# Optimization experiments

Hardware: AMD Instinct MI355X
Metric: run time of the kernel (lower is better)

The kernel has to match this reference:

```python
import jax, jax.numpy as jnp
import numpy as np


def _pointnet(x, w1, b1, w2, b2, w3, b3):
    # x: [B, 3, P]; shared per-point MLP 3->64->128->128, max-pool over points -> [B,128]
    h = jax.nn.relu(jnp.einsum('oc,bcp->bop', w1, x) + b1[None, :, None])
    h = jax.nn.relu(jnp.einsum('oc,bcp->bop', w2, h) + b2[None, :, None])
    h = jax.nn.relu(jnp.einsum('oc,bcp->bop', w3, h) + b3[None, :, None])
    return h.max(axis=2)


def _lstm_layer(x, wih, whh, b):
    # x: [B, T, D]; standard LSTM (pytorch gate order i,f,g,o), returns [B, T, 128]
    B = x.shape[0]
    h0 = jnp.zeros((B, 128), x.dtype)
    def step(carry, xt):
        h, c = carry
        g = xt @ wih.T + h @ whh.T + b
        i, f, gg, o = jnp.split(g, 4, axis=-1)
        c = jax.nn.sigmoid(f) * c + jax.nn.sigmoid(i) * jnp.tanh(gg)
        h = jax.nn.sigmoid(o) * jnp.tanh(c)
        return (h, c), h
    _, hs = jax.lax.scan(step, (h0, h0), jnp.swapaxes(x, 0, 1))
    return jnp.swapaxes(hs, 0, 1)


def _edgeconv(x, aff, tw, tb, pw, pb, N):
    # DGL EdgeConv, max aggregation. Edges: det i -> track (N+j) where aff[i,j]==1, plus
    # self loops on every node. Message on edge u->v: theta(x_u - x_v) + phi(x_v).
    phi = x @ pw.T + pb                                   # [N+M, 256]
    diff = x[:N][:, None, :] - x[N:][None, :, :]          # [N, M, 256] (x_src - x_dst)
    msg = jnp.einsum('nmc,oc->nmo', diff, tw) + tb        # theta applied to diffs
    msg = jnp.where(aff[:, :, None] > 0, msg, jnp.finfo(x.dtype).min)
    h_trk = phi[N:] + jnp.maximum(tb, msg.max(axis=0))    # self-loop message is theta(0)=tb
    h_det = phi[:N] + tb                                  # dets only receive their self loop
    return jnp.concatenate([h_det, h_trk], axis=0)


def _forward(det_pc_in_box, det_boxes3d, track_pc_in_box, track_boxes3d, init_aff_matrix,
             pn_w1, pn_b1, pn_w2, pn_b2, pn_w3, pn_b3,
             mlp_w1, mlp_b1, mlp_w2, mlp_b2,
             l0_wih, l0_whh, l0_b, l1_wih, l1_whh, l1_b,
             ec_tw, ec_tb, ec_pw, ec_pb,
             er_w1, er_b1, er_w2, er_b2):
    N = det_pc_in_box.shape[0]
    det_app = _pointnet(jnp.swapaxes(det_pc_in_box, 1, 2), pn_w1, pn_b1, pn_w2, pn_b2, pn_w3, pn_b3)
    trk_app = _pointnet(jnp.swapaxes(track_pc_in_box, 1, 2), pn_w1, pn_b1, pn_w2, pn_b2, pn_w3, pn_b3)
    det_mot = jax.nn.relu(det_boxes3d @ mlp_w1.T + mlp_b1) @ mlp_w2.T + mlp_b2
    trk_mot = _lstm_layer(_lstm_layer(track_boxes3d, l0_wih, l0_whh, l0_b), l1_wih, l1_whh, l1_b)[:, -1, :]
    h = jnp.concatenate([jnp.concatenate([det_app, det_mot], axis=1),
                         jnp.concatenate([trk_app, trk_mot], axis=1)], axis=0)  # [N+M, 256]
    for k in range(4):
        h = jax.nn.relu(_edgeconv(h, init_aff_matrix, ec_tw[k], ec_tb[k], ec_pw[k], ec_pb[k], N))
    # pairwise affinity: (track - det) differences through small MLP + sigmoid (BCE head)
    edges = h[N:][None, :, :] - h[:N][:, None, :]                                # [N, M, 256]
    e = jax.nn.relu(jnp.einsum('nmc,oc->nmo', edges, er_w1) + er_b1)             # [N, M, 64]
    regr = jax.nn.sigmoid(jnp.einsum('nmo,ko->nmk', e, er_w2) + er_b2)[..., 0]   # [N, M]
    valid = init_aff_matrix * regr
    valid = jnp.where(valid == 0, jnp.asarray(99.0, valid.dtype), valid)
    return valid


def setup_inputs() -> dict:
    key = jax.random.key(0)
    ks = jax.random.split(key, 20)
    N, M, P, T = 512, 512, 256, 10
    f = jnp.float32
    def rn(k, shp):
        return jax.random.normal(k, shp, dtype=f) * 0.05
    return {
        'det_pc_in_box': jax.random.normal(ks[0], (N, P, 3), dtype=f),
        'det_boxes3d': jax.random.normal(ks[1], (N, 9), dtype=f),
        'track_pc_in_box': jax.random.normal(ks[2], (M, P, 3), dtype=f),
        'track_boxes3d': jax.random.normal(ks[3], (M, T, 9), dtype=f),
        'init_aff_matrix': jnp.ones((N, M), dtype=f),
        'gt_affinity_matrix': jnp.zeros((N, M), dtype=jnp.int32),
        'pn_w1': rn(ks[4], (64, 3)), 'pn_b1': jnp.zeros((64,), f),
        'pn_w2': rn(ks[5], (128, 64)), 'pn_b2': jnp.zeros((128,), f),
        'pn_w3': rn(ks[6], (128, 128)), 'pn_b3': jnp.zeros((128,), f),
        'mlp_w1': rn(ks[7], (64, 9)), 'mlp_b1': jnp.zeros((64,), f),
        'mlp_w2': rn(ks[8], (128, 64)), 'mlp_b2': jnp.zeros((128,), f),
        'l0_wih': rn(ks[9], (512, 9)), 'l0_whh': rn(ks[10], (512, 128)), 'l0_b': jnp.zeros((512,), f),
        'l1_wih': rn(ks[11], (512, 128)), 'l1_whh': rn(ks[12], (512, 128)), 'l1_b': jnp.zeros((512,), f),
        'ec_tw': rn(ks[13], (4, 256, 256)), 'ec_tb': jnp.zeros((4, 256), f),
        'ec_pw': rn(ks[14], (4, 256, 256)), 'ec_pb': jnp.zeros((4, 256), f),
        'er_w1': rn(ks[15], (64, 256)), 'er_b1': jnp.zeros((64,), f),
        'er_w2': rn(ks[16], (1, 64)), 'er_b2': jnp.zeros((1,), f),
    }


def reference(det_pc_in_box, det_boxes3d, track_pc_in_box, track_boxes3d, init_aff_matrix,
              gt_affinity_matrix,
              pn_w1, pn_b1, pn_w2, pn_b2, pn_w3, pn_b3,
              mlp_w1, mlp_b1, mlp_w2, mlp_b2,
              l0_wih, l0_whh, l0_b, l1_wih, l1_whh, l1_b,
              ec_tw, ec_tb, ec_pw, ec_pb,
              er_w1, er_b1, er_w2, er_b2):
    # gt_affinity_matrix is only used by the training loss; inference path ignores it.
    return _forward(det_pc_in_box, det_boxes3d, track_pc_in_box, track_boxes3d, init_aff_matrix,
                    pn_w1, pn_b1, pn_w2, pn_b2, pn_w3, pn_b3,
                    mlp_w1, mlp_b1, mlp_w2, mlp_b2,
                    l0_wih, l0_whh, l0_b, l1_wih, l1_whh, l1_b,
                    ec_tw, ec_tb, ec_pw, ec_pb,
                    er_w1, er_b1, er_w2, er_b2)
```

## Files before the change

kernel.cpp:

```cpp
#include <hip/hip_runtime.h>
#include <math.h>

#define N_DET 512
#define N_TRK 512
#define NPTS  256

typedef __attribute__((ext_vector_type(8))) short short8;
typedef __attribute__((ext_vector_type(4))) float f32x4;

__device__ __forceinline__ float sigm(float x) { return 1.f / (1.f + expf(-x)); }

__device__ __forceinline__ unsigned short f2bf(float f) {
    unsigned u = __float_as_uint(f);
    u += 0x7FFF + ((u >> 16) & 1);
    return (unsigned short)(u >> 16);
}

__global__ __launch_bounds__(64) void pn_wprep_kernel(
    const float* __restrict__ w2, const float* __restrict__ w3,
    unsigned short* __restrict__ wfrag)
{
    const int f = blockIdx.x;
    const int lane = threadIdx.x;
    const int lm = lane & 15, lg = lane >> 4;
    const float* src;
    if (f < 16) {
        const int s = f >> 3, n = f & 7;
        src = w2 + (size_t)(n*16 + lm)*64 + s*32 + lg*8;
    } else {
        const int f2 = f - 16, s = f2 >> 3, n = f2 & 7;
        src = w3 + (size_t)(n*16 + lm)*128 + s*32 + lg*8;
    }
    short8 v;
#pragma unroll
    for (int j = 0; j < 8; ++j) v[j] = (short)f2bf(src[j]);
    *reinterpret_cast<short8*>(wfrag + ((size_t)f*64 + lane)*8) = v;
}

__global__ __launch_bounds__(256, 1) void pointnet_mfma_kernel(
    const float* __restrict__ det_pc, const float* __restrict__ trk_pc,
    const float* __restrict__ w1, const float* __restrict__ b1,
    const unsigned short* __restrict__ wfrag,
    const float* __restrict__ b2, const float* __restrict__ b3,
    float* __restrict__ hout)
{
    __shared__ unsigned short h1s[256*72];
    __shared__ unsigned short h2s[256*136];
    __shared__ float wmaxs[4][128];

    const int tid = threadIdx.x;
    const int box = blockIdx.x;
    const int lane = tid & 63, w = tid >> 6;
    const int lm = lane & 15, lg = lane >> 4;

    const float* pc = (box < N_DET) ? det_pc + ((size_t)box*NPTS + tid)*3
                                    : trk_pc + ((size_t)(box - N_DET)*NPTS + tid)*3;
    const float x = pc[0], y = pc[1], z = pc[2];
#pragma unroll
    for (int j = 0; j < 8; ++j) {
        short8 v;
#pragma unroll
        for (int o = 0; o < 8; ++o) {
            const int ch = j*8 + o;
            float s = fmaf(w1[ch*3+0], x, fmaf(w1[ch*3+1], y,
                        fmaf(w1[ch*3+2], z, b1[ch])));
            v[o] = (short)f2bf(fmaxf(s, 0.f));
        }
        *reinterpret_cast<short8*>(&h1s[tid*72 + j*8]) = v;
    }
    __syncthreads();

    short8 w2f[16];
#pragma unroll
    for (int f = 0; f < 16; ++f)
        w2f[f] = *reinterpret_cast<const short8*>(wfrag + ((size_t)f*64 + lane)*8);
    float b2v[8];
#pragma unroll
    for (int n = 0; n < 8; ++n) b2v[n] = b2[n*16 + lm];

#pragma unroll
    for (int t = 0; t < 4; ++t) {
        const int arow = w*64 + t*16 + lm;
        const short8 a0 = *reinterpret_cast<const short8*>(&h1s[arow*72 + lg*8]);
        const short8 a1 = *reinterpret_cast<const short8*>(&h1s[arow*72 + 32 + lg*8]);
        const int wrow = w*64 + t*16 + lg*4;
#pragma unroll
        for (int n = 0; n < 8; ++n) {
            f32x4 acc = {0.f, 0.f, 0.f, 0.f};
            acc = __builtin_amdgcn_mfma_f32_16x16x32_bf16(a0, w2f[n],     acc, 0, 0, 0);
            acc = __builtin_amdgcn_mfma_f32_16x16x32_bf16(a1, w2f[8 + n], acc, 0, 0, 0);
#pragma unroll
            for (int r = 0; r < 4; ++r) {
                const float v = fmaxf(acc[r] + b2v[n], 0.f);
                h2s[(wrow + r)*136 + n*16 + lm] = f2bf(v);
            }
        }
    }
    __syncthreads();

    short8 w3f[32];
#pragma unroll
    for (int f = 0; f < 32; ++f)
        w3f[f] = *reinterpret_cast<const short8*>(wfrag + ((size_t)(16 + f)*64 + lane)*8);

    float pm[8];
#pragma unroll
    for (int n = 0; n < 8; ++n) pm[n] = -3.0e38f;

#pragma unroll
    for (int t = 0; t < 4; ++t) {
        const int arow = w*64 + t*16 + lm;
        const short8 a0 = *reinterpret_cast<const short8*>(&h2s[arow*136 +  0 + lg*8]);
        const short8 a1 = *reinterpret_cast<const short8*>(&h2s[arow*136 + 32 + lg*8]);
        const short8 a2 = *reinterpret_cast<const short8*>(&h2s[arow*136 + 64 + lg*8]);
        const short8 a3 = *reinterpret_cast<const short8*>(&h2s[arow*136 + 96 + lg*8]);
#pragma unroll
        for (int n = 0; n < 8; ++n) {
            f32x4 acc = {0.f, 0.f, 0.f, 0.f};
            acc = __builtin_amdgcn_mfma_f32_16x16x32_bf16(a0, w3f[n],      acc, 0, 0, 0);
            acc = __builtin_amdgcn_mfma_f32_16x16x32_bf16(a1, w3f[8 + n],  acc, 0, 0, 0);
            acc = __builtin_amdgcn_mfma_f32_16x16x32_bf16(a2, w3f[16 + n], acc, 0, 0, 0);
            acc = __builtin_amdgcn_mfma_f32_16x16x32_bf16(a3, w3f[24 + n], acc, 0, 0, 0);
#pragma unroll
            for (int r = 0; r < 4; ++r) pm[n] = fmaxf(pm[n], acc[r]);
        }
    }
#pragma unroll
    for (int n = 0; n < 8; ++n) {
        float v = pm[n];
        v = fmaxf(v, __shfl_xor(v, 16, 64));
        v = fmaxf(v, __shfl_xor(v, 32, 64));
        pm[n] = v;
    }
    if (lg == 0) {
#pragma unroll
        for (int n = 0; n < 8; ++n) wmaxs[w][n*16 + lm] = pm[n];
    }
    __syncthreads();
    if (tid < 128) {
        const float m = fmaxf(fmaxf(wmaxs[0][tid], wmaxs[1][tid]),
                              fmaxf(wmaxs[2][tid], wmaxs[3][tid]));
        hout[(size_t)box*256 + tid] = fmaxf(m + b3[tid], 0.f);
    }
}

__global__ __launch_bounds__(128) void detmlp_kernel(
    const float* __restrict__ boxes,
    const float* __restrict__ w1, const float* __restrict__ b1,
    const float* __restrict__ w2, const float* __restrict__ b2,
    float* __restrict__ hout)
{
    __shared__ float xb[9];
    __shared__ float h1[64];
    const int b = blockIdx.x, t = threadIdx.x;
    if (t < 9) xb[t] = boxes[b*9 + t];
    __syncthreads();
    if (t < 64) {
        float s = b1[t];
#pragma unroll
        for (int c = 0; c < 9; ++c) s = fmaf(w1[t*9+c], xb[c], s);
        h1[t] = fmaxf(s, 0.f);
    }
    __syncthreads();
    float s = b2[t];
    const float* wr = w2 + t*64;
#pragma unroll
    for (int c = 0; c < 64; ++c) s = fmaf(wr[c], h1[c], s);
    hout[(size_t)b * 256 + 128 + t] = s;
}

__global__ __launch_bounds__(256) void transpose_wih1_kernel(
    const float* __restrict__ in, float* __restrict__ out)
{
    const int id = blockIdx.x * 256 + threadIdx.x;
    const int k = id >> 9, r = id & 511;
    out[id] = in[r * 128 + k];
}

__global__ __launch_bounds__(512) void lstm_rec0_kernel(
    const float* __restrict__ xseq,
    const float* __restrict__ wih0, const float* __restrict__ whh0,
    const float* __restrict__ b0, float* __restrict__ h0seq)
{
    __shared__ float hs[128][2];
    __shared__ float xb[2][12];
    __shared__ float gs[4][2][128];
    const int r  = threadIdx.x;
    const int b2 = blockIdx.x * 2;
    const int q  = r >> 7 & 3, jj = r & 127;
    const int mb = r >> 7, mj = r & 127;

    float w[128];
#pragma unroll
    for (int k = 0; k < 128; k += 4) {
        const float4 v = *(const float4*)(whh0 + (size_t)r * 128 + k);
        w[k] = v.x; w[k+1] = v.y; w[k+2] = v.z; w[k+3] = v.w;
    }
    float wx[9];
#pragma unroll
    for (int c = 0; c < 9; ++c) wx[c] = wih0[(size_t)r * 9 + c];
    const float bias = b0[r];

    float cst = 0.f;
    if (r < 256) hs[mj][mb] = 0.f;
    __syncthreads();

    for (int t = 0; t < 10; ++t) {
        if (r < 18) xb[r / 9][r % 9] = xseq[((size_t)(b2 + r / 9) * 10 + t) * 9 + r % 9];
        __syncthreads();
        float a0 = bias, a1 = bias;
#pragma unroll
        for (int c = 0; c < 9; ++c) {
            a0 = fmaf(wx[c], xb[0][c], a0);
            a1 = fmaf(wx[c], xb[1][c], a1);
        }
#pragma unroll
        for (int k = 0; k < 128; ++k) {
            const float2 h2 = *(const float2*)&hs[k][0];
            a0 = fmaf(w[k], h2.x, a0);
            a1 = fmaf(w[k], h2.y, a1);
        }
        gs[q][0][jj] = a0;
        gs[q][1][jj] = a1;
        __syncthreads();
        if (r < 256) {
            const float gi = gs[0][mb][mj], gf = gs[1][mb][mj];
            const float gg = gs[2][mb][mj], go = gs[3][mb][mj];
            cst = sigm(gf) * cst + sigm(gi) * tanhf(gg);
            const float hn = sigm(go) * tanhf(cst);
            hs[mj][mb] = hn;
            h0seq[((size_t)(b2 + mb) * 10 + t) * 128 + mj] = hn;
        }
        __syncthreads();
    }
}

__global__ __launch_bounds__(512) void lstm_rec1_kernel(
    const float* __restrict__ h0seq, const float* __restrict__ wih1T,
    const float* __restrict__ whh1, const float* __restrict__ b1,
    float* __restrict__ hout)
{
    __shared__ float hs[128][2];
    __shared__ float xs_[128][2];
    __shared__ float gs[4][2][128];
    const int r  = threadIdx.x;
    const int b2 = blockIdx.x * 2;
    const int q  = r >> 7 & 3, jj = r & 127;
    const int mb = r >> 7, mj = r & 127;

    float w[128];
#pragma unroll
    for (int k = 0; k < 128; k += 4) {
        const float4 v = *(const float4*)(whh1 + (size_t)r * 128 + k);
        w[k] = v.x; w[k+1] = v.y; w[k+2] = v.z; w[k+3] = v.w;
    }
    const float bias = b1[r];

    float cst = 0.f;
    if (r < 256) hs[mj][mb] = 0.f;
    __syncthreads();

    for (int t = 0; t < 10; ++t) {
        if (r < 256)
            xs_[mj][mb] = h0seq[((size_t)(b2 + mb) * 10 + t) * 128 + mj];
        __syncthreads();
        float a0 = bias, a1 = bias;
#pragma unroll
        for (int k = 0; k < 128; ++k) {
            const float wxv = wih1T[k * 512 + r];
            const float2 x2 = *(const float2*)&xs_[k][0];
            const float2 h2 = *(const float2*)&hs[k][0];
            a0 = fmaf(wxv, x2.x, fmaf(w[k], h2.x, a0));
            a1 = fmaf(wxv, x2.y, fmaf(w[k], h2.y, a1));
        }
        gs[q][0][jj] = a0;
        gs[q][1][jj] = a1;
        __syncthreads();
        if (r < 256) {
            const float gi = gs[0][mb][mj], gf = gs[1][mb][mj];
            const float gg = gs[2][mb][mj], go = gs[3][mb][mj];
            cst = sigm(gf) * cst + sigm(gi) * tanhf(gg);
            const float hn = sigm(go) * tanhf(cst);
            hs[mj][mb] = hn;
            if (t == 9)
                hout[(size_t)(N_DET + b2 + mb) * 256 + 128 + mj] = hn;
        }
        __syncthreads();
    }
}

__global__ __launch_bounds__(256) void ec_gemm_kernel(
    const float* __restrict__ hin,
    const float* __restrict__ tw, const float* __restrict__ tb,
    const float* __restrict__ pw, const float* __restrict__ pb,
    float* __restrict__ Abuf, float* __restrict__ Bbuf,
    float* __restrict__ phiT, float* __restrict__ hnext)
{
    __shared__ float As[16][68];
    __shared__ float Ws[16][68];
    const int bm = blockIdx.x, bn = blockIdx.y;
    const int tid = threadIdx.x;
    const int tx = tid & 15, ty = tid >> 4;
    float acc[4][4] = {};
    for (int kk = 0; kk < 256; kk += 16) {
        if (kk) __syncthreads();
#pragma unroll
        for (int i = 0; i < 4; ++i) {
            const int e = tid + 256*i;
            const int r = e >> 4, c = e & 15;
            As[c][r] = hin[(size_t)(bm*64 + r)*256 + kk + c];
            const int n = bn*64 + r;
            const float* wp = (n < 256) ? (tw + (size_t)n*256) : (pw + (size_t)(n-256)*256);
            Ws[c][r] = wp[kk + c];
        }
        __syncthreads();
#pragma unroll
        for (int k = 0; k < 16; ++k) {
            const float4 a = *(const float4*)&As[k][ty*4];
            const float4 w = *(const float4*)&Ws[k][tx*4];
            const float av[4] = {a.x, a.y, a.z, a.w};
            const float wv[4] = {w.x, w.y, w.z, w.w};
#pragma unroll
            for (int i = 0; i < 4; ++i)
#pragma unroll
                for (int jj = 0; jj < 4; ++jj)
                    acc[i][jj] = fmaf(av[i], wv[jj], acc[i][jj]);
        }
    }
    const int row0 = bm*64 + ty*4;
    const int col0 = bn*64 + tx*4;
#pragma unroll
    for (int i = 0; i < 4; ++i) {
#pragma unroll
        for (int jj = 0; jj < 4; ++jj) {
            const int row = row0 + i, col = col0 + jj;
            float v = acc[i][jj];
            if (col < 256) {
                if (row < N_DET) Abuf[(size_t)row*256 + col] = v;
                else             Bbuf[(size_t)(row - N_DET)*256 + col] = v;
            } else {
                const int o = col - 256;
                v += pb[o];
                if (row < N_DET) hnext[(size_t)row*256 + o] = fmaxf(v + tb[o], 0.f);
                else             phiT[(size_t)(row - N_DET)*256 + o] = v;
            }
        }
    }
}

#define CM_MT 16
#define CM_OT 32
#define CM_NC 64

__global__ __launch_bounds__(256) void ec_colmax_kernel(
    const float* __restrict__ aff,
    const float* __restrict__ Abuf, const float* __restrict__ Bbuf,
    const float* __restrict__ phiT, const float* __restrict__ tb,
    float* __restrict__ hnext)
{
    __shared__ float As[CM_NC][CM_OT + 4];
    __shared__ float Fs[CM_NC][CM_MT + 4];
    const int t = threadIdx.x;
    const int mtile = blockIdx.x;
    const int otile = blockIdx.y;
    const int mi = t >> 4, oi = t & 15;

    float mx0 = -3.0e38f, mx1 = -3.0e38f;

    for (int n0 = 0; n0 < 512; n0 += CM_NC) {
        if (n0) __syncthreads();
        {
            const int r = t >> 3, c4 = (t & 7) * 4;
#pragma unroll
            for (int rr = 0; rr < 2; ++rr) {
                const float4 v = *(const float4*)(
                    Abuf + (size_t)(n0 + rr*32 + r)*256 + otile*CM_OT + c4);
                *(float4*)&As[rr*32 + r][c4] = v;
            }
        }
        {
            const int n = t >> 2, m4 = (t & 3) * 4;
            const float4 a = *(const float4*)(
                aff + (size_t)(n0 + n)*512 + mtile*CM_MT + m4);
            float4 f;
            f.x = (a.x > 0.f) ? 0.f : -3.0e38f;
            f.y = (a.y > 0.f) ? 0.f : -3.0e38f;
            f.z = (a.z > 0.f) ? 0.f : -3.0e38f;
            f.w = (a.w > 0.f) ? 0.f : -3.0e38f;
            *(float4*)&Fs[n][m4] = f;
        }
        __syncthreads();
#pragma unroll 4
        for (int n = 0; n < CM_NC; ++n) {
            const float f = Fs[n][mi];
            const float2 a = *(const float2*)&As[n][oi*2];
            mx0 = fmaxf(mx0, a.x + f);
            mx1 = fmaxf(mx1, a.y + f);
        }
    }

    const int m = mtile*CM_MT + mi;
    const int o = otile*CM_OT + oi*2;
    const float2 tb2 = *(const float2*)(tb + o);
    const float2 bb  = *(const float2*)(Bbuf + (size_t)m*256 + o);
    const float2 ph  = *(const float2*)(phiT + (size_t)m*256 + o);
    const float v0 = fmaxf(tb2.x, mx0 - bb.x + tb2.x);
    const float v1 = fmaxf(tb2.y, mx1 - bb.y + tb2.y);
    float2 outv;
    outv.x = fmaxf(ph.x + v0, 0.f);
    outv.y = fmaxf(ph.y + v1, 0.f);
    *(float2*)(hnext + (size_t)(N_DET + m)*256 + o) = outv;
}

__global__ __launch_bounds__(256) void headp_kernel(
    const float* __restrict__ h, const float* __restrict__ w1, float* __restrict__ P)
{
    const int tid = threadIdx.x;
    const int o = tid & 63, rl = tid >> 6;
    const int row = blockIdx.x * 4 + rl;
    const float* hr = h + (size_t)row * 256;
    const float* wr = w1 + (size_t)o * 256;
    float s0 = 0.f, s1 = 0.f, s2 = 0.f, s3 = 0.f;
#pragma unroll
    for (int c = 0; c < 256; c += 4) {
        const float4 hv = *(const float4*)(hr + c);
        const float4 wv = *(const float4*)(wr + c);
        s0 = fmaf(hv.x, wv.x, s0);
        s1 = fmaf(hv.y, wv.y, s1);
        s2 = fmaf(hv.z, wv.z, s2);
        s3 = fmaf(hv.w, wv.w, s3);
    }
    P[(size_t)row * 64 + o] = (s0 + s1) + (s2 + s3);
}

__global__ __launch_bounds__(256) void pairwise_kernel(
    const float* __restrict__ P, const float* __restrict__ aff,
    const float* __restrict__ eb1, const float* __restrict__ ew2, const float* __restrict__ eb2,
    float* __restrict__ out)
{
    __shared__ float pd[64], sb1[64], sw2[64];
    const int n = blockIdx.y;
    const int t = threadIdx.x;
    if (t < 64)       pd[t]        = P[(size_t)n * 64 + t];
    else if (t < 128) sb1[t - 64]  = eb1[t - 64];
    else if (t < 192) sw2[t - 128] = ew2[t - 128];
    __syncthreads();
    const int m = blockIdx.x * 256 + t;
    const float* pt = P + (size_t)(N_DET + m) * 64;
    float s = eb2[0];
#pragma unroll
    for (int c = 0; c < 64; c += 4) {
        const float4 pv = *(const float4*)(pt + c);
        float e;
        e = fmaxf(pv.x - pd[c+0] + sb1[c+0], 0.f); s = fmaf(e, sw2[c+0], s);
        e = fmaxf(pv.y - pd[c+1] + sb1[c+1], 0.f); s = fmaf(e, sw2[c+1], s);
        e = fmaxf(pv.z - pd[c+2] + sb1[c+2], 0.f); s = fmaf(e, sw2[c+2], s);
        e = fmaxf(pv.w - pd[c+3] + sb1[c+3], 0.f); s = fmaf(e, sw2[c+3], s);
    }
    const float r = 1.f / (1.f + expf(-s));
    const float v = aff[(size_t)n * 512 + m] * r;
    out[(size_t)n * 512 + m] = (v == 0.f) ? 99.f : v;
}

extern "C" void kernel_launch(void* const* d_in, const int* in_sizes, int n_in,
                              void* d_out, int out_size, void* d_ws, size_t ws_size,
                              hipStream_t stream)
{
    (void)in_sizes; (void)n_in; (void)out_size; (void)ws_size;

    const float* det_pc  = (const float*)d_in[0];
    const float* det_box = (const float*)d_in[1];
    const float* trk_pc  = (const float*)d_in[2];
    const float* trk_box = (const float*)d_in[3];
    const float* aff     = (const float*)d_in[4];
    const float* pn_w1  = (const float*)d_in[6];
    const float* pn_b1  = (const float*)d_in[7];
    const float* pn_w2  = (const float*)d_in[8];
    const float* pn_b2  = (const float*)d_in[9];
    const float* pn_w3  = (const float*)d_in[10];
    const float* pn_b3  = (const float*)d_in[11];
    const float* mlp_w1 = (const float*)d_in[12];
    const float* mlp_b1 = (const float*)d_in[13];
    const float* mlp_w2 = (const float*)d_in[14];
    const float* mlp_b2 = (const float*)d_in[15];
    const float* l0_wih = (const float*)d_in[16];
    const float* l0_whh = (const float*)d_in[17];
    const float* l0_b   = (const float*)d_in[18];
    const float* l1_wih = (const float*)d_in[19];
    const float* l1_whh = (const float*)d_in[20];
    const float* l1_b   = (const float*)d_in[21];
    const float* ec_tw  = (const float*)d_in[22];
    const float* ec_tb  = (const float*)d_in[23];
    const float* ec_pw  = (const float*)d_in[24];
    const float* ec_pb  = (const float*)d_in[25];
    const float* er_w1  = (const float*)d_in[26];
    const float* er_b1  = (const float*)d_in[27];
    const float* er_w2  = (const float*)d_in[28];
    const float* er_b2  = (const float*)d_in[29];

    float* ws    = (float*)d_ws;
    float* hA    = ws;
    float* hB    = hA + 1024*256;
    float* Abuf  = hB + 1024*256;
    float* Bbuf  = Abuf + 512*256;
    float* phiT  = Bbuf + 512*256;
    float* P     = phiT + 512*256;
    float* h0seq = P + 1024*64;
    float* wih1T = h0seq + 512*10*128;
    unsigned short* wfrag = (unsigned short*)(wih1T + 128*512);

    pn_wprep_kernel<<<48, 64, 0, stream>>>(pn_w2, pn_w3, wfrag);
    pointnet_mfma_kernel<<<1024, 256, 0, stream>>>(det_pc, trk_pc, pn_w1, pn_b1,
                                                   wfrag, pn_b2, pn_b3, hA);
    detmlp_kernel<<<512, 128, 0, stream>>>(det_box, mlp_w1, mlp_b1, mlp_w2, mlp_b2, hA);
    transpose_wih1_kernel<<<256, 256, 0, stream>>>(l1_wih, wih1T);
    lstm_rec0_kernel<<<256, 512, 0, stream>>>(trk_box, l0_wih, l0_whh, l0_b, h0seq);
    lstm_rec1_kernel<<<256, 512, 0, stream>>>(h0seq, wih1T, l1_whh, l1_b, hA);

    float* hcur = hA;
    float* hnext = hB;
    for (int k = 0; k < 4; ++k) {
        const float* tw = ec_tw + (size_t)k * 256 * 256;
        const float* tb = ec_tb + (size_t)k * 256;
        const float* pw = ec_pw + (size_t)k * 256 * 256;
        const float* pb = ec_pb + (size_t)k * 256;
        ec_gemm_kernel<<<dim3(16, 8), 256, 0, stream>>>(hcur, tw, tb, pw, pb,
                                                        Abuf, Bbuf, phiT, hnext);
        ec_colmax_kernel<<<dim3(32, 8), 256, 0, stream>>>(aff, Abuf, Bbuf, phiT, tb, hnext);
        float* tmp = hcur; hcur = hnext; hnext = tmp;
    }

    headp_kernel<<<256, 256, 0, stream>>>(hcur, er_w1, P);
    pairwise_kernel<<<dim3(2, 512), 256, 0, stream>>>(P, aff, er_b1, er_w2, er_b2,
                                                      (float*)d_out);
}
```

Baseline: 413.8 us.

## Move EdgeConv GEMM onto bf16 MFMA with split hi/lo precision

```diff
diff --git a/kernel.cpp b/kernel.cpp
--- a/kernel.cpp
+++ b/kernel.cpp
@@ -7,6 +7,7 @@
 
 typedef __attribute__((ext_vector_type(8))) short short8;
 typedef __attribute__((ext_vector_type(4))) float f32x4;
+typedef unsigned short ushort_t;
 
 __device__ __forceinline__ float sigm(float x) { return 1.f / (1.f + expf(-x)); }
 
@@ -14,6 +15,9 @@
     unsigned u = __float_as_uint(f);
     u += 0x7FFF + ((u >> 16) & 1);
     return (unsigned short)(u >> 16);
+}
+__device__ __forceinline__ float bf2f(unsigned short h) {
+    return __uint_as_float(((unsigned)h) << 16);
 }
 
 __global__ __launch_bounds__(64) void pn_wprep_kernel(
@@ -35,6 +39,49 @@
 #pragma unroll
     for (int j = 0; j < 8; ++j) v[j] = (short)f2bf(src[j]);
     *reinterpret_cast<short8*>(wfrag + ((size_t)f*64 + lane)*8) = v;
+}
+
+__global__ __launch_bounds__(64) void ec_wprep_kernel(
+    const float* __restrict__ tw, const float* __restrict__ pw,
+    unsigned short* __restrict__ whi, unsigned short* __restrict__ wlo)
+{
+    const int id = blockIdx.x;
+    const int layer = id >> 8;
+    const int ntile = (id >> 3) & 31, kf = id & 7;
+    const int lane = threadIdx.x;
+    const int lm = lane & 15, lg = lane >> 4;
+    const int col = ntile*16 + lm, k = kf*32 + lg*8;
+    const float* src = (col < 256)
+        ? tw + ((size_t)layer*256 + col)*256 + k
+        : pw + ((size_t)layer*256 + (col - 256))*256 + k;
+    short8 hi, lo;
+#pragma unroll
+    for (int j = 0; j < 8; ++j) {
+        const float f = src[j];
+        const unsigned short h = f2bf(f);
+        hi[j] = (short)h;
+        lo[j] = (short)f2bf(f - bf2f(h));
+    }
+    const size_t off = ((size_t)id*64 + lane)*8;
+    *reinterpret_cast<short8*>(whi + off) = hi;
+    *reinterpret_cast<short8*>(wlo + off) = lo;
+}
+
+__global__ __launch_bounds__(256) void h2bf_kernel(
+    const float* __restrict__ h,
+    unsigned short* __restrict__ hi, unsigned short* __restrict__ lo)
+{
+    const int id = blockIdx.x * 256 + threadIdx.x;
+    const float4 v = *(const float4*)(h + (size_t)id*4);
+    ushort_t h4[4], l4[4];
+    const float vv[4] = {v.x, v.y, v.z, v.w};
+#pragma unroll
+    for (int j = 0; j < 4; ++j) {
+        h4[j] = f2bf(vv[j]);
+        l4[j] = f2bf(vv[j] - bf2f(h4[j]));
+    }
+    *(ulong1*)(hi + (size_t)id*4) = *(ulong1*)h4;
+    *(ulong1*)(lo + (size_t)id*4) = *(ulong1*)l4;
 }
 
 __global__ __launch_bounds__(256, 1) void pointnet_mfma_kernel(
@@ -289,60 +336,62 @@
     }
 }
 
-__global__ __launch_bounds__(256) void ec_gemm_kernel(
-    const float* __restrict__ hin,
-    const float* __restrict__ tw, const float* __restrict__ tb,
-    const float* __restrict__ pw, const float* __restrict__ pb,
+__global__ __launch_bounds__(256) void ec_gemm_mfma_kernel(
+    const unsigned short* __restrict__ hhi, const unsigned short* __restrict__ hlo,
+    const unsigned short* __restrict__ whi, const unsigned short* __restrict__ wlo,
+    const float* __restrict__ tb, const float* __restrict__ pb,
     float* __restrict__ Abuf, float* __restrict__ Bbuf,
-    float* __restrict__ phiT, float* __restrict__ hnext)
-{
-    __shared__ float As[16][68];
-    __shared__ float Ws[16][68];
+    float* __restrict__ phiT, float* __restrict__ hnext,
+    unsigned short* __restrict__ nhi, unsigned short* __restrict__ nlo)
+{
     const int bm = blockIdx.x, bn = blockIdx.y;
-    const int tid = threadIdx.x;
-    const int tx = tid & 15, ty = tid >> 4;
-    float acc[4][4] = {};
-    for (int kk = 0; kk < 256; kk += 16) {
-        if (kk) __syncthreads();
-#pragma unroll
-        for (int i = 0; i < 4; ++i) {
-            const int e = tid + 256*i;
-            const int r = e >> 4, c = e & 15;
-            As[c][r] = hin[(size_t)(bm*64 + r)*256 + kk + c];
-            const int n = bn*64 + r;
-            const float* wp = (n < 256) ? (tw + (size_t)n*256) : (pw + (size_t)(n-256)*256);
-            Ws[c][r] = wp[kk + c];
-        }
-        __syncthreads();
-#pragma unroll
-        for (int k = 0; k < 16; ++k) {
-            const float4 a = *(const float4*)&As[k][ty*4];
-            const float4 w = *(const float4*)&Ws[k][tx*4];
-            const float av[4] = {a.x, a.y, a.z, a.w};
-            const float wv[4] = {w.x, w.y, w.z, w.w};
-#pragma unroll
-            for (int i = 0; i < 4; ++i)
-#pragma unroll
-                for (int jj = 0; jj < 4; ++jj)
-                    acc[i][jj] = fmaf(av[i], wv[jj], acc[i][jj]);
-        }
-    }
-    const int row0 = bm*64 + ty*4;
-    const int col0 = bn*64 + tx*4;
-#pragma unroll
-    for (int i = 0; i < 4; ++i) {
-#pragma unroll
-        for (int jj = 0; jj < 4; ++jj) {
-            const int row = row0 + i, col = col0 + jj;
-            float v = acc[i][jj];
+    const int tid = threadIdx.x, lane = tid & 63, w = tid >> 6;
+    const int lm = lane & 15, lg = lane >> 4;
+    const int mrow0 = bm*32 + (w & 1)*16;
+    const int nt0   = bn*4 + (w >> 1)*2;
+    const int arow  = mrow0 + lm;
+
+    f32x4 acc[2] = {{0.f,0.f,0.f,0.f},{0.f,0.f,0.f,0.f}};
+
+#pragma unroll
+    for (int kf = 0; kf < 8; ++kf) {
+        const short8 ahi = *reinterpret_cast<const short8*>(
+            hhi + (size_t)arow*256 + kf*32 + lg*8);
+        const short8 alo = *reinterpret_cast<const short8*>(
+            hlo + (size_t)arow*256 + kf*32 + lg*8);
+#pragma unroll
+        for (int n2 = 0; n2 < 2; ++n2) {
+            const size_t foff = ((size_t)((nt0 + n2)*8 + kf)*64 + lane)*8;
+            const short8 bhi = *reinterpret_cast<const short8*>(whi + foff);
+            const short8 blo = *reinterpret_cast<const short8*>(wlo + foff);
+            acc[n2] = __builtin_amdgcn_mfma_f32_16x16x32_bf16(ahi, bhi, acc[n2], 0, 0, 0);
+            acc[n2] = __builtin_amdgcn_mfma_f32_16x16x32_bf16(alo, bhi, acc[n2], 0, 0, 0);
+            acc[n2] = __builtin_amdgcn_mfma_f32_16x16x32_bf16(ahi, blo, acc[n2], 0, 0, 0);
+        }
+    }
+
+#pragma unroll
+    for (int n2 = 0; n2 < 2; ++n2) {
+        const int col = (nt0 + n2)*16 + lm;
+#pragma unroll
+        for (int r = 0; r < 4; ++r) {
+            const int row = mrow0 + lg*4 + r;
+            float v = acc[n2][r];
             if (col < 256) {
                 if (row < N_DET) Abuf[(size_t)row*256 + col] = v;
                 else             Bbuf[(size_t)(row - N_DET)*256 + col] = v;
             } else {
                 const int o = col - 256;
                 v += pb[o];
-                if (row < N_DET) hnext[(size_t)row*256 + o] = fmaxf(v + tb[o], 0.f);
-                else             phiT[(size_t)(row - N_DET)*256 + o] = v;
+                if (row < N_DET) {
+                    const float hv = fmaxf(v + tb[o], 0.f);
+                    hnext[(size_t)row*256 + o] = hv;
+                    const unsigned short hb = f2bf(hv);
+                    nhi[(size_t)row*256 + o] = hb;
+                    nlo[(size_t)row*256 + o] = f2bf(hv - bf2f(hb));
+                } else {
+                    phiT[(size_t)(row - N_DET)*256 + o] = v;
+                }
             }
         }
     }
@@ -356,7 +405,8 @@
     const float* __restrict__ aff,
     const float* __restrict__ Abuf, const float* __restrict__ Bbuf,
     const float* __restrict__ phiT, const float* __restrict__ tb,
-    float* __restrict__ hnext)
+    float* __restrict__ hnext,
+    unsigned short* __restrict__ nhi, unsigned short* __restrict__ nlo)
 {
     __shared__ float As[CM_NC][CM_OT + 4];
     __shared__ float Fs[CM_NC][CM_MT + 4];
@@ -409,7 +459,13 @@
     float2 outv;
     outv.x = fmaxf(ph.x + v0, 0.f);
     outv.y = fmaxf(ph.y + v1, 0.f);
-    *(float2*)(hnext + (size_t)(N_DET + m)*256 + o) = outv;
+    const size_t base = (size_t)(N_DET + m)*256 + o;
+    *(float2*)(hnext + base) = outv;
+    const unsigned short h0 = f2bf(outv.x), h1 = f2bf(outv.y);
+    nhi[base]     = h0;
+    nhi[base + 1] = h1;
+    nlo[base]     = f2bf(outv.x - bf2f(h0));
+    nlo[base + 1] = f2bf(outv.y - bf2f(h1));
 }
 
 __global__ __launch_bounds__(256) void headp_kernel(
@@ -508,26 +564,37 @@
     float* h0seq = P + 1024*64;
     float* wih1T = h0seq + 512*10*128;
     unsigned short* wfrag = (unsigned short*)(wih1T + 128*512);
+    unsigned short* ecwhi = wfrag + 48*64*8;
+    unsigned short* ecwlo = ecwhi + 1024*64*8;
+    unsigned short* hbfA_hi = ecwlo + 1024*64*8;
+    unsigned short* hbfA_lo = hbfA_hi + 1024*256;
+    unsigned short* hbfB_hi = hbfA_lo + 1024*256;
+    unsigned short* hbfB_lo = hbfB_hi + 1024*256;
 
     pn_wprep_kernel<<<48, 64, 0, stream>>>(pn_w2, pn_w3, wfrag);
+    ec_wprep_kernel<<<1024, 64, 0, stream>>>(ec_tw, ec_pw, ecwhi, ecwlo);
     pointnet_mfma_kernel<<<1024, 256, 0, stream>>>(det_pc, trk_pc, pn_w1, pn_b1,
                                                    wfrag, pn_b2, pn_b3, hA);
     detmlp_kernel<<<512, 128, 0, stream>>>(det_box, mlp_w1, mlp_b1, mlp_w2, mlp_b2, hA);
     transpose_wih1_kernel<<<256, 256, 0, stream>>>(l1_wih, wih1T);
     lstm_rec0_kernel<<<256, 512, 0, stream>>>(trk_box, l0_wih, l0_whh, l0_b, h0seq);
     lstm_rec1_kernel<<<256, 512, 0, stream>>>(h0seq, wih1T, l1_whh, l1_b, hA);
-
-    float* hcur = hA;
-    float* hnext = hB;
+    h2bf_kernel<<<256, 256, 0, stream>>>(hA, hbfA_hi, hbfA_lo);
+
+    float* hcur = hA;  float* hnext = hB;
+    unsigned short* chi = hbfA_hi; unsigned short* clo = hbfA_lo;
+    unsigned short* nhi = hbfB_hi; unsigned short* nlo = hbfB_lo;
     for (int k = 0; k < 4; ++k) {
-        const float* tw = ec_tw + (size_t)k * 256 * 256;
         const float* tb = ec_tb + (size_t)k * 256;
-        const float* pw = ec_pw + (size_t)k * 256 * 256;
         const float* pb = ec_pb + (size_t)k * 256;
-        ec_gemm_kernel<<<dim3(16, 8), 256, 0, stream>>>(hcur, tw, tb, pw, pb,
-                                                        Abuf, Bbuf, phiT, hnext);
-        ec_colmax_kernel<<<dim3(32, 8), 256, 0, stream>>>(aff, Abuf, Bbuf, phiT, tb, hnext);
-        float* tmp = hcur; hcur = hnext; hnext = tmp;
+        ec_gemm_mfma_kernel<<<dim3(32, 8), 256, 0, stream>>>(
+            chi, clo, ecwhi + (size_t)k*256*64*8, ecwlo + (size_t)k*256*64*8,
+            tb, pb, Abuf, Bbuf, phiT, hnext, nhi, nlo);
+        ec_colmax_kernel<<<dim3(32, 8), 256, 0, stream>>>(aff, Abuf, Bbuf, phiT, tb,
+                                                          hnext, nhi, nlo);
+        float* tf = hcur; hcur = hnext; hnext = tf;
+        unsigned short* th = chi; chi = nhi; nhi = th;
+        unsigned short* tl = clo; clo = nlo; nlo = tl;
     }
 
     headp_kernel<<<256, 256, 0, stream>>>(hcur, er_w1, P);
```

After: 382.5 us. 7.6% less time.
